# Optimization experiments

Measured on AMD Instinct MI355X. Metric: run time of the kernel, lower is better.

Reference implementation:

```python
import jax, jax.numpy as jnp
import numpy as np

BS = 8
SP_IN, DN_IN = 256, 128
SP_OUT, DN_OUT = 512, 256
N_STK, N_STK_PNT = 32, 64
COOR = 64
SP_NEAR, DN_NEAR = 2, 10
BN_EPS = 1e-5


def _act(x):
    return jax.nn.leaky_relu(x, 0.2)


def _bn(x, g, b, axes):
    # training-mode batch norm over `axes`, per channel (axis 1)
    m = x.mean(axes, keepdims=True)
    v = x.var(axes, keepdims=True)
    shp = [1] * x.ndim
    shp[1] = x.shape[1]
    return g.reshape(shp) * (x - m) * jax.lax.rsqrt(v + BN_EPS) + b.reshape(shp)


def _conv2d(x, w, b, stride, pad_w):
    # x [B,C,H,W], w [O,I,1,kw]
    y = jax.lax.conv_general_dilated(
        x, w, window_strides=stride, padding=[(0, 0), (pad_w, pad_w)],
        dimension_numbers=('NCHW', 'OIHW', 'NCHW'))
    return y + b[None, :, None, None]


def _sq_dist(a, b):
    # a [B,N,C], b [B,M,C] -> [B,N,M]
    return (jnp.sum(a * a, -1)[:, :, None] + jnp.sum(b * b, -1)[:, None, :]
            - 2.0 * jnp.einsum('bnc,bmc->bnm', a, b))


def _index_points(p, idx):
    # p [B,N,C], idx [B,...] -> [B,...,C]
    B = p.shape[0]
    bidx = jnp.arange(B).reshape((B,) + (1,) * (idx.ndim - 1))
    return p[bidx, idx]


def _fps(x, m):
    # deterministic farthest point sampling, start at index 0. x [B,N,D] -> [B,m]
    B, N, _ = x.shape
    bar = jnp.arange(B)

    def step(carry, _):
        dist, far = carry
        cen = x[bar, far]                       # [B,D]
        d = jnp.sum((x - cen[:, None, :]) ** 2, -1)
        dist = jnp.minimum(dist, d)
        return (dist, jnp.argmax(dist, -1).astype(jnp.int32)), far

    init = (jnp.full((B, N), 1e10, x.dtype), jnp.zeros((B,), jnp.int32))
    _, idx = jax.lax.scan(step, init, None, length=m)
    return idx.T  # [B,m]


def _gcn(x, W, b, g, be, k):
    # DGCNN-style EdgeConv: knn in feature space, edge feat [x_j - x_i, x_i],
    # shared 1x1 conv + BN + act, max over neighbors. x [B,C,N] -> [B,O,N]
    xt = jnp.transpose(x, (0, 2, 1))            # [B,N,C]
    d = _sq_dist(xt, xt)
    _, idx = jax.lax.top_k(-d, k)               # [B,N,k] (includes self)
    neigh = _index_points(xt, idx)              # [B,N,k,C]
    cen = xt[:, :, None, :]
    edge = jnp.concatenate([neigh - cen, jnp.broadcast_to(cen, neigh.shape)], -1)
    h = jnp.einsum('bnkc,oc->bonk', edge, W) + b[None, :, None, None]
    h = _act(_bn(h, g, be, (0, 2, 3)))
    return jnp.max(h, axis=3)                   # [B,O,N]


def _forward(sparse_fea, dense_fea, stk_coor,
             d2s_w, d2s_b, d2s_g, d2s_be,
             gsp_w, gsp_b, gsp_g, gsp_be,
             gdn_w, gdn_b, gdn_g, gdn_be,
             dcv_w, dcv_b, dcv_g, dcv_be):
    bs = sparse_fea.shape[0]
    dn4 = dense_fea.reshape(bs, DN_IN, N_STK, N_STK_PNT)

    # DenseToSparse: conv (1,3) valid, BN, act, max over points -> concat
    h = _act(_bn(_conv2d(dn4, d2s_w, d2s_b, (1, 1), 0), d2s_g, d2s_be, (0, 2, 3)))
    sp_from_dn = jnp.max(h, axis=3)                       # [bs,DN_IN,N_STK]
    union_sparse = jnp.concatenate([sparse_fea, sp_from_dn], 1)

    # SparseToDense: broadcast stroke feature onto its points -> concat
    dn_from_sp = jnp.repeat(sparse_fea[:, :, :, None], N_STK_PNT, axis=3)
    union_dense = jnp.concatenate([dn4, dn_from_sp], 1).reshape(
        bs, SP_IN + DN_IN, N_STK * N_STK_PNT)

    # graph updates
    union_sparse = _gcn(union_sparse, gsp_w, gsp_b, gsp_g, gsp_be, SP_NEAR)   # [bs,SP_OUT,N_STK]
    union_dense = _gcn(union_dense, gdn_w, gdn_b, gdn_g, gdn_be, DN_NEAR)     # [bs,DN_OUT,N_pnt]

    # DownSample: FPS over strokes, gather, strided conv halves point count
    fps_idx = _fps(stk_coor, N_STK // 2)                  # [bs,N_STK//2]
    stk_coor_s = _index_points(stk_coor, fps_idx)         # [bs,N_STK//2,COOR]
    sp = jnp.transpose(_index_points(jnp.transpose(union_sparse, (0, 2, 1)), fps_idx), (0, 2, 1))

    emb_d = union_dense.shape[1]
    dn = union_dense.reshape(bs, emb_d, N_STK, N_STK_PNT).transpose(0, 2, 3, 1)
    dn = dn.reshape(bs, N_STK, N_STK_PNT * emb_d)
    dn = _index_points(dn, fps_idx)                       # gather whole strokes
    dn = dn.reshape(bs, N_STK // 2, N_STK_PNT, emb_d).transpose(0, 3, 1, 2)
    dn = _act(_bn(_conv2d(dn, dcv_w, dcv_b, (1, 2), 1), dcv_g, dcv_be, (0, 2, 3)))
    dn = dn.reshape(bs, dn.shape[1], (N_STK // 2) * (N_STK_PNT // 2))
    return sp, dn, stk_coor_s


def setup_inputs() -> dict:
    key = jax.random.key(0)
    ks = jax.random.split(key, 8)
    C_u = SP_IN + DN_IN

    def rn(k, shape, s=0.05):
        return jax.random.normal(k, shape, jnp.float32) * s

    return {
        'sparse_fea': jax.random.normal(ks[0], (BS, SP_IN, N_STK), jnp.float32),
        'dense_fea': jax.random.normal(ks[1], (BS, DN_IN, N_STK * N_STK_PNT), jnp.float32),
        'stk_coor': jax.random.normal(ks[2], (BS, N_STK, COOR), jnp.float32),
        'd2s_w': rn(ks[3], (DN_IN, DN_IN, 1, 3)), 'd2s_b': jnp.zeros(DN_IN),
        'd2s_g': jnp.ones(DN_IN), 'd2s_be': jnp.zeros(DN_IN),
        'gsp_w': rn(ks[4], (SP_OUT, 2 * C_u)), 'gsp_b': jnp.zeros(SP_OUT),
        'gsp_g': jnp.ones(SP_OUT), 'gsp_be': jnp.zeros(SP_OUT),
        'gdn_w': rn(ks[5], (DN_OUT, 2 * C_u)), 'gdn_b': jnp.zeros(DN_OUT),
        'gdn_g': jnp.ones(DN_OUT), 'gdn_be': jnp.zeros(DN_OUT),
        'dcv_w': rn(ks[6], (DN_OUT, DN_OUT, 1, 3)), 'dcv_b': jnp.zeros(DN_OUT),
        'dcv_g': jnp.ones(DN_OUT), 'dcv_be': jnp.zeros(DN_OUT),
    }


def reference(sparse_fea, dense_fea, stk_coor,
              d2s_w, d2s_b, d2s_g, d2s_be,
              gsp_w, gsp_b, gsp_g, gsp_be,
              gdn_w, gdn_b, gdn_g, gdn_be,
              dcv_w, dcv_b, dcv_g, dcv_be):
    return _forward(sparse_fea, dense_fea, stk_coor,
                    d2s_w, d2s_b, d2s_g, d2s_be,
                    gsp_w, gsp_b, gsp_g, gsp_be,
                    gdn_w, gdn_b, gdn_g, gdn_be,
                    dcv_w, dcv_b, dcv_g, dcv_be)
```

## Files before the change

kernel.cpp:

```cpp
#include <hip/hip_runtime.h>

#define NPTS 2048
#define CUF 384

__device__ __forceinline__ float lrelu(float y){ return y>=0.f ? y : 0.2f*y; }

#define GLD16(g, l) __builtin_amdgcn_global_load_lds( \
    (const __attribute__((address_space(1))) void*)(g), \
    (__attribute__((address_space(3))) void*)(l), 16, 0, 0)

__global__ void k_build_xdn(const float* __restrict__ dense,
                            const float* __restrict__ sparse,
                            float* __restrict__ X){
  int b = blockIdx.y, ch = blockIdx.x;
  int t = threadIdx.x;
  __shared__ float tile[64*128];
  for (int k=0;k<32;k++){
    int f = t + k*256;
    int c = f>>6, j = f&63;
    tile[j*128 + c] = dense[((size_t)b*128 + c)*NPTS + ch*64 + j];
  }
  __syncthreads();
  for (int k=0;k<32;k++){
    int f = t + k*256;
    int j = f>>7, c = f&127;
    X[((size_t)b*NPTS + ch*64 + j)*CUF + c] = tile[f];
  }
  float v = sparse[((size_t)b*256 + t)*32 + ch];
  for (int j=0;j<64;j++) X[((size_t)b*NPTS + ch*64 + j)*CUF + 128 + t] = v;
}

__global__ void k_sn(const float* __restrict__ X, float* __restrict__ sn){
  int g = blockIdx.x*256 + threadIdx.x;
  if (g >= 8*NPTS) return;
  const float* row = X + (size_t)g*CUF;
  float blk[4];
  #pragma unroll
  for (int bI=0;bI<4;bI++){
    const float* p = row + bI*96;
    float r[8];
    #pragma unroll
    for (int l=0;l<8;l++) r[l] = __fmul_rn(p[l], p[l]);
    #pragma unroll 1
    for (int i=8;i<96;i+=8){
      #pragma unroll
      for (int l=0;l<8;l++) r[l] = __fadd_rn(r[l], __fmul_rn(p[i+l], p[i+l]));
    }
    float s01 = __fadd_rn(r[0], r[1]);
    float s23 = __fadd_rn(r[2], r[3]);
    float s45 = __fadd_rn(r[4], r[5]);
    float s67 = __fadd_rn(r[6], r[7]);
    blk[bI] = __fadd_rn(__fadd_rn(s01, s23), __fadd_rn(s45, s67));
  }
  sn[g] = __fadd_rn(__fadd_rn(blk[0], blk[1]), __fadd_rn(blk[2], blk[3]));
}

__global__ __launch_bounds__(256) void k_dist_tri(
    const float* __restrict__ X, float* __restrict__ Dot, int b_base){
  int z = blockIdx.z; int b = b_base + z;
  int t = threadIdx.x;
  int tx = t & 15, ty = t >> 4;
  int idx = blockIdx.x, rb = 0;
  while (idx >= 16 - rb){ idx -= 16 - rb; rb++; }
  int cb = rb + idx;
  __shared__ float U[8448];
  float* Xr = U;
  float* Xc = U + 4096;
  float* Ds = U;
  int r0 = rb*128;
  int c0 = cb*128;
  const size_t xb = (size_t)b*NPTS*CUF;
  const size_t zb = (size_t)z*NPTS*NPTS;

  int wv  = t >> 6;
  int sub = (t & 63) >> 3;
  int gs  = t & 7;
  int rowsA[4]; int swzA[4];
  #pragma unroll
  for (int cc=0;cc<4;cc++){
    int grp = wv*4 + cc;
    int row = grp*8 + sub;
    rowsA[cc] = row;
    swzA[cc] = 4*(gs ^ (row&7));
  }

  float acc[8][8];
  #pragma unroll
  for (int i=0;i<8;i++){
    #pragma unroll
    for (int j=0;j<8;j++) acc[i][j] = 0.f;
  }
  for (int kt=0; kt<12; kt++){
    int k0 = kt*32;
    __syncthreads();
    #pragma unroll
    for (int cc=0;cc<4;cc++){
      int grp = wv*4 + cc;
      GLD16(X + xb + (size_t)(r0+rowsA[cc])*CUF + k0 + swzA[cc], Xr + grp*256);
      GLD16(X + xb + (size_t)(c0+rowsA[cc])*CUF + k0 + swzA[cc], Xc + grp*256);
    }
    __syncthreads();
    #pragma unroll
    for (int kk=0; kk<32; kk+=4){
      int G = kk>>2;
      float4 aa[8], bb[8];
      #pragma unroll
      for (int i=0;i<8;i++){ int r = ty+16*i; aa[i] = *(const float4*)&Xr[r*32 + 4*(G ^ (r&7))]; }
      #pragma unroll
      for (int j=0;j<8;j++){ int r = tx+16*j; bb[j] = *(const float4*)&Xc[r*32 + 4*(G ^ (r&7))]; }
      #pragma unroll
      for (int i=0;i<8;i++){
        #pragma unroll
        for (int j=0;j<8;j++){
          float a_ = acc[i][j];
          a_ = fmaf(aa[i].x, bb[j].x, a_);
          a_ = fmaf(aa[i].y, bb[j].y, a_);
          a_ = fmaf(aa[i].z, bb[j].z, a_);
          a_ = fmaf(aa[i].w, bb[j].w, a_);
          acc[i][j] = a_;
        }
      }
    }
  }
  #pragma unroll
  for (int i=0;i<8;i++){
    size_t rbase = zb + (size_t)(r0 + ty + 16*i)*NPTS + c0;
    #pragma unroll
    for (int j=0;j<8;j++) Dot[rbase + tx + 16*j] = acc[i][j];
  }
  if (rb != cb){
    for (int h=0; h<2; h++){
      __syncthreads();
      #pragma unroll
      for (int i2=0;i2<4;i2++){
        #pragma unroll
        for (int j=0;j<8;j++){
          Ds[(tx+16*j)*65 + ty + 16*i2] = acc[h*4+i2][j];
        }
      }
      __syncthreads();
      for (int e=t; e<128*64; e+=256){
        int col = e>>6, rr = e&63;
        Dot[zb + (size_t)(c0+col)*NPTS + r0 + h*64 + rr] = Ds[col*65 + rr];
      }
    }
  }
}

__global__ __launch_bounds__(256) void k_sel(const float* __restrict__ Dot,
                                             const float* __restrict__ sn,
                                             int* __restrict__ idx, int b_base){
  int t = threadIdx.x;
  int lane = t & 63, w = t >> 6;
  int rglob = blockIdx.x*4 + w;
  int bb = rglob >> 11;
  int r  = rglob & 2047;
  int b  = b_base + bb;
  const float* drow = Dot + ((size_t)bb*NPTS + r)*NPTS;
  const float* snp  = sn + (size_t)b*NPTS;
  float snr = snp[r];
  unsigned long long key[32];
  #pragma unroll
  for (int k=0;k<8;k++){
    int cbase = k*256 + lane*4;
    float4 dd = *(const float4*)&drow[cbase];
    float4 ss = *(const float4*)&snp[cbase];
    float v0 = __fsub_rn(__fadd_rn(snr, ss.x), __fmul_rn(2.0f, dd.x));
    float v1 = __fsub_rn(__fadd_rn(snr, ss.y), __fmul_rn(2.0f, dd.y));
    float v2 = __fsub_rn(__fadd_rn(snr, ss.z), __fmul_rn(2.0f, dd.z));
    float v3 = __fsub_rn(__fadd_rn(snr, ss.w), __fmul_rn(2.0f, dd.w));
    float vv[4] = {v0, v1, v2, v3};
    #pragma unroll
    for (int u=0;u<4;u++){
      unsigned int bits = __float_as_uint(vv[u]);
      unsigned int flip = bits ^ ((unsigned int)((int)bits >> 31) | 0x80000000u);
      key[k*4+u] = ((unsigned long long)flip << 32) | (unsigned int)(cbase + u);
    }
  }
  unsigned long long last = 0ull;
  int out[10];
  #pragma unroll
  for (int q=0;q<10;q++){
    const unsigned long long INF = 0xFFFFFFFFFFFFFFFFull;
    unsigned long long m0[16];
    #pragma unroll
    for (int s=0;s<16;s++){
      unsigned long long a = (key[s]    > last) ? key[s]    : INF;
      unsigned long long c = (key[s+16] > last) ? key[s+16] : INF;
      m0[s] = (c < a) ? c : a;
    }
    #pragma unroll
    for (int s=0;s<8;s++) m0[s] = (m0[s+8] < m0[s]) ? m0[s+8] : m0[s];
    #pragma unroll
    for (int s=0;s<4;s++) m0[s] = (m0[s+4] < m0[s]) ? m0[s+4] : m0[s];
    m0[0] = (m0[2] < m0[0]) ? m0[2] : m0[0];
    m0[1] = (m0[3] < m0[1]) ? m0[3] : m0[1];
    unsigned long long m = (m0[1] < m0[0]) ? m0[1] : m0[0];
    #pragma unroll
    for (int sh=1; sh<64; sh<<=1){
      unsigned long long o = (unsigned long long)__shfl_xor((long long)m, sh, 64);
      m = (o < m) ? o : m;
    }
    last = m;
    out[q] = (int)(m & 0xFFFFFFFFull);
  }
  if (lane == 0){
    int* o = idx + ((size_t)b*NPTS + r)*10;
    #pragma unroll
    for (int q=0;q<10;q++) o[q] = out[q];
  }
}

__global__ void k_prepw(const float* __restrict__ Wsrc, float* __restrict__ Wcat, int Ohalf){
  int g = blockIdx.x*256 + threadIdx.x;
  int total = Ohalf*2*CUF;
  if (g >= total) return;
  int o = g / CUF, c = g % CUF;
  float v;
  if (o < Ohalf) v = Wsrc[(size_t)o*768 + c];
  else { int oo = o - Ohalf; v = Wsrc[(size_t)oo*768 + 384 + c] - Wsrc[(size_t)oo*768 + c]; }
  Wcat[g] = v;
}

__global__ __launch_bounds__(256) void k_gemm_pq2(const float* __restrict__ A, const float* __restrict__ W,
                         const float* __restrict__ bias, float* __restrict__ OUT){
  int b = blockIdx.z, mb = blockIdx.y, ob = blockIdx.x;
  int t = threadIdx.x; int tx = t&15, ty = t>>4;
  __shared__ float Xa[4096];
  __shared__ float Xw[4096];
  int m0 = mb*128, o0 = ob*128;
  float acc[8][8];
  #pragma unroll
  for (int i=0;i<8;i++){
    #pragma unroll
    for (int j=0;j<8;j++) acc[i][j] = 0.f;
  }
  int wv  = t >> 6;
  int sub = (t & 63) >> 3;
  int gs  = t & 7;
  int rowsA[4]; int swzA[4];
  #pragma unroll
  for (int cc=0;cc<4;cc++){
    int grp = wv*4 + cc;
    int row = grp*8 + sub;
    rowsA[cc] = row;
    swzA[cc] = 4*(gs ^ (row&7));
  }
  for (int kt=0; kt<12; kt++){
    int k0 = kt*32;
    __syncthreads();
    #pragma unroll
    for (int cc=0;cc<4;cc++){
      int grp = wv*4 + cc;
      GLD16(A + ((size_t)b*NPTS + m0 + rowsA[cc])*CUF + k0 + swzA[cc], Xa + grp*256);
      GLD16(W + (size_t)(o0 + rowsA[cc])*CUF + k0 + swzA[cc], Xw + grp*256);
    }
    __syncthreads();
    #pragma unroll
    for (int kk=0; kk<32; kk+=4){
      int G = kk>>2;
      float4 aa[8], bb[8];
      #pragma unroll
      for (int i=0;i<8;i++){ int r = ty+16*i; aa[i] = *(const float4*)&Xa[r*32 + 4*(G ^ (r&7))]; }
      #pragma unroll
      for (int j=0;j<8;j++){ int r = tx+16*j; bb[j] = *(const float4*)&Xw[r*32 + 4*(G ^ (r&7))]; }
      #pragma unroll
      for (int i=0;i<8;i++){
        #pragma unroll
        for (int j=0;j<8;j++){
          float a_ = acc[i][j];
          a_ = fmaf(aa[i].x, bb[j].x, a_);
          a_ = fmaf(aa[i].y, bb[j].y, a_);
          a_ = fmaf(aa[i].z, bb[j].z, a_);
          a_ = fmaf(aa[i].w, bb[j].w, a_);
          acc[i][j] = a_;
        }
      }
    }
  }
  #pragma unroll
  for (int i=0;i<8;i++){
    int m = m0 + ty + 16*i;
    #pragma unroll
    for (int j=0;j<8;j++){
      int o = o0 + tx + 16*j;
      float v = acc[i][j];
      if (o >= 256) v += bias[o - 256];
      OUT[((size_t)b*NPTS + m)*512 + o] = v;
    }
  }
}

__global__ __launch_bounds__(256) void k_gemm_pq(const float* __restrict__ A, const float* __restrict__ W,
                         const float* __restrict__ bias,
                         float* __restrict__ OUT, int M, int Ototal, int Ohalf){
  int b = blockIdx.z, mb = blockIdx.y, ob = blockIdx.x;
  int t = threadIdx.x; int tr = t&15, tc = t>>4;
  __shared__ float At[64][68], Wt[64][68];
  int m0 = mb*64, o0 = ob*64;
  float acc[4][4];
  #pragma unroll
  for(int i=0;i<4;i++){
    #pragma unroll
    for(int j=0;j<4;j++) acc[i][j]=0.f;
  }
  int li = t>>2, lk = (t&3)*16;
  for (int kt=0;kt<6;kt++){
    int k0 = kt*64;
    {
      int m = m0 + li;
      if (m < M){
        const float4* p = (const float4*)(A + ((size_t)b*M + m)*CUF + k0 + lk);
        #pragma unroll
        for (int e=0;e<4;e++) *(float4*)&At[li][lk+e*4] = p[e];
      } else {
        float4 z = make_float4(0.f,0.f,0.f,0.f);
        #pragma unroll
        for (int e=0;e<4;e++) *(float4*)&At[li][lk+e*4] = z;
      }
      const float4* pw = (const float4*)(W + (size_t)(o0+li)*CUF + k0 + lk);
      #pragma unroll
      for (int e=0;e<4;e++) *(float4*)&Wt[li][lk+e*4] = pw[e];
    }
    __syncthreads();
    #pragma unroll
    for (int k4=0;k4<16;k4++){
      float4 aa[4], bb[4];
      aa[0] = *(const float4*)&At[tr   ][k4*4];
      aa[1] = *(const float4*)&At[tr+16][k4*4];
      aa[2] = *(const float4*)&At[tr+32][k4*4];
      aa[3] = *(const float4*)&At[tr+48][k4*4];
      bb[0] = *(const float4*)&Wt[tc   ][k4*4];
      bb[1] = *(const float4*)&Wt[tc+16][k4*4];
      bb[2] = *(const float4*)&Wt[tc+32][k4*4];
      bb[3] = *(const float4*)&Wt[tc+48][k4*4];
      #pragma unroll
      for(int i=0;i<4;i++){
        #pragma unroll
        for(int j=0;j<4;j++)
          acc[i][j] += aa[i].x*bb[j].x + aa[i].y*bb[j].y + aa[i].z*bb[j].z + aa[i].w*bb[j].w;
      }
    }
    __syncthreads();
  }
  #pragma unroll
  for(int i=0;i<4;i++){
    int m = m0 + tr + 16*i;
    if (m < M){
      #pragma unroll
      for(int j=0;j<4;j++){
        int o = o0 + tc + 16*j;
        float v = acc[i][j];
        if (o >= Ohalf) v += bias[o - Ohalf];
        OUT[((size_t)b*M + m)*Ototal + o] = v;
      }
    }
  }
}

__global__ __launch_bounds__(256) void k_gather_dn(const float* __restrict__ PQ, const int* __restrict__ idx,
                            float* __restrict__ dmax, float* __restrict__ dmin, double* __restrict__ part){
  int b = blockIdx.y, nb = blockIdx.x; int t = threadIdx.x;
  __shared__ int sidx[640];
  int n0 = nb*64;
  for (int k=t; k<640; k+=256) sidx[k] = idx[((size_t)b*NPTS + n0)*10 + k] & 2047;
  __syncthreads();
  double s=0.0, s2=0.0;
  const size_t pb = (size_t)b*NPTS*512;
  for (int n=0;n<64;n++){
    float qv = PQ[pb + (size_t)(n0+n)*512 + 256 + t];
    float mx = -3.4e38f, mn = 3.4e38f;
    #pragma unroll
    for (int k=0;k<10;k++){
      int m = sidx[n*10+k];
      float h = PQ[pb + (size_t)m*512 + t] + qv;
      mx = fmaxf(mx,h); mn = fminf(mn,h);
      s += h; s2 += (double)h*(double)h;
    }
    dmax[((size_t)b*NPTS + n0+n)*256 + t] = mx;
    dmin[((size_t)b*NPTS + n0+n)*256 + t] = mn;
  }
  size_t blk = (size_t)b*32 + nb;
  part[(blk*256 + t)*2] = s; part[(blk*256 + t)*2+1] = s2;
}

__global__ void k_reduce(const double* __restrict__ part, float* __restrict__ mv,
                         int nblk, int C, int count){
  int c = blockIdx.x; int t = threadIdx.x;
  double s=0.0, s2=0.0;
  for (int k=t;k<nblk;k+=64){ s += part[((size_t)k*C+c)*2]; s2 += part[((size_t)k*C+c)*2+1]; }
  #pragma unroll
  for (int off=32; off>=1; off>>=1){ s += __shfl_down(s, off, 64); s2 += __shfl_down(s2, off, 64); }
  if (t==0){
    double mean = s / (double)count;
    double var = s2 / (double)count - mean*mean;
    mv[c*2] = (float)mean;
    mv[c*2+1] = (float)(1.0 / sqrt(var + 1e-5));
  }
}

__global__ void k_epi(const float* __restrict__ xmin, float* __restrict__ xmax,
                      const float* __restrict__ mv, const float* __restrict__ g,
                      const float* __restrict__ be, int C, size_t total){
  size_t i = (size_t)blockIdx.x*256 + threadIdx.x;
  if (i>=total) return;
  int c = (int)(i % (size_t)C);
  float gg = g[c];
  float x = gg >= 0.f ? xmax[i] : xmin[i];
  float y = gg*(x - mv[c*2])*mv[c*2+1] + be[c];
  xmax[i] = lrelu(y);
}

__global__ __launch_bounds__(128) void k_d2s(const float* __restrict__ dense,
                      const float* __restrict__ w, const float* __restrict__ bias,
                      float* __restrict__ mx, float* __restrict__ mn, double* __restrict__ part){
  int b = blockIdx.y, s = blockIdx.x; int t = threadIdx.x;
  __shared__ float IN[128*64];
  for (int k=0;k<64;k++){
    int f = t + k*128;
    int ci = f>>6, wj = f&63;
    IN[f] = dense[((size_t)b*128 + ci)*NPTS + s*64 + wj];
  }
  __syncthreads();
  float acc[62];
  float bv = bias[t];
  #pragma unroll
  for (int wj=0;wj<62;wj++) acc[wj]=bv;
  for (int ci=0;ci<128;ci++){
    const float* wp = w + ((size_t)t*128 + ci)*3;
    float w0 = wp[0], w1 = wp[1], w2 = wp[2];
    const float* row = &IN[ci*64];
    #pragma unroll
    for (int wj=0;wj<62;wj++) acc[wj] += row[wj]*w0 + row[wj+1]*w1 + row[wj+2]*w2;
  }
  float vmx=-3.4e38f, vmn=3.4e38f; double ss=0.0, ss2=0.0;
  #pragma unroll
  for (int wj=0;wj<62;wj++){ float v = acc[wj]; vmx=fmaxf(vmx,v); vmn=fminf(vmn,v); ss+=v; ss2+=(double)v*(double)v; }
  mx[((size_t)b*32+s)*128 + t] = vmx;
  mn[((size_t)b*32+s)*128 + t] = vmn;
  part[(((size_t)b*32+s)*128 + t)*2] = ss; part[(((size_t)b*32+s)*128 + t)*2+1] = ss2;
}

__global__ void k_build_xs(const float* __restrict__ sparse,
                           const float* __restrict__ mx, const float* __restrict__ mn,
                           const float* __restrict__ mv, const float* __restrict__ g,
                           const float* __restrict__ be, float* __restrict__ Xs){
  int b = blockIdx.x; int c = threadIdx.x;
  for (int n=0;n<32;n++){
    float v;
    if (c < 256) v = sparse[((size_t)b*256 + c)*32 + n];
    else {
      int cc = c-256;
      float gg = g[cc];
      float x = gg>=0.f ? mx[((size_t)b*32+n)*128+cc] : mn[((size_t)b*32+n)*128+cc];
      v = lrelu(gg*(x - mv[cc*2])*mv[cc*2+1] + be[cc]);
    }
    Xs[((size_t)b*32+n)*384 + c] = v;
  }
}

__global__ __launch_bounds__(256) void k_knn_sp(const float* __restrict__ Xs, int* __restrict__ idx){
  int b = blockIdx.x; int t = threadIdx.x;
  __shared__ float Xh[32*388];
  __shared__ float snl[32];
  __shared__ float D[32*33];
  for (int k=t;k<32*384;k+=256){ int n=k/384, c=k-n*384; Xh[n*388+c] = Xs[(size_t)b*32*384 + k]; }
  __syncthreads();
  if (t<32){ double s=0.0; for (int c=0;c<384;c++){ double v=(double)Xh[t*388+c]; s+=v*v; } snl[t]=(float)s; }
  __syncthreads();
  for (int p=t;p<1024;p+=256){
    int n=p>>5, m=p&31;
    const float* A=&Xh[n*388]; const float* B=&Xh[m*388];
    double s=0.0;
    for (int c=0;c<384;c++) s += (double)A[c]*(double)B[c];
    D[n*33+m] = (float)((double)snl[m] - 2.0*s);
  }
  __syncthreads();
  if (t<32){
    float v0=3.4e38f,v1=3.4e38f; int i0=0,i1=0;
    for (int m=0;m<32;m++){
      float v=D[t*33+m];
      if (v < v0){ v1=v0;i1=i0; v0=v;i0=m; }
      else if (v < v1){ v1=v;i1=m; }
    }
    idx[((size_t)b*32+t)*2]=i0; idx[((size_t)b*32+t)*2+1]=i1;
  }
}

__global__ void k_gather_sp(const float* __restrict__ PQ, const int* __restrict__ idx,
                            float* __restrict__ umax, float* __restrict__ umin, double* __restrict__ part){
  int b = blockIdx.x; int t = threadIdx.x;
  double s=0.0, s2=0.0;
  for (int n=0;n<32;n++){
    float qv = PQ[((size_t)b*32+n)*1024 + 512 + t];
    float mxv=-3.4e38f, mnv=3.4e38f;
    #pragma unroll
    for (int k=0;k<2;k++){
      int m = idx[((size_t)b*32+n)*2+k] & 31;
      float h = PQ[((size_t)b*32+m)*1024 + t] + qv;
      mxv=fmaxf(mxv,h); mnv=fminf(mnv,h); s+=h; s2+=(double)h*(double)h;
    }
    umax[((size_t)b*32+n)*512+t]=mxv; umin[((size_t)b*32+n)*512+t]=mnv;
  }
  part[((size_t)b*512+t)*2]=s; part[((size_t)b*512+t)*2+1]=s2;
}

__global__ void k_fps(const float* __restrict__ coor, int* __restrict__ fps){
  int b = blockIdx.x; int t = threadIdx.x;
  __shared__ float C[32*64]; __shared__ float dist[32]; __shared__ int fs;
  for (int k=t;k<2048;k+=64) C[k] = coor[(size_t)b*2048 + k];
  if (t<32) dist[t]=1e10f;
  if (t==0) fs=0;
  __syncthreads();
  for (int it=0; it<16; it++){
    int f = fs;
    if (t==0) fps[b*16+it] = f;
    if (t<32){
      float d=0.f;
      for (int c=0;c<64;c++){ float df = C[t*64+c]-C[f*64+c]; d += df*df; }
      dist[t] = fminf(dist[t], d);
    }
    __syncthreads();
    if (t==0){
      float bd=-1.f; int bi=0;
      for (int n=0;n<32;n++){ if (dist[n]>bd){bd=dist[n];bi=n;} }
      fs=bi;
    }
    __syncthreads();
  }
}

__global__ void k_out0(const float* __restrict__ usp, const int* __restrict__ fps, float* __restrict__ out0){
  int b = blockIdx.y, s = blockIdx.x; int t = threadIdx.x;
  int n = fps[b*16+s] & 31;
  out0[((size_t)b*512 + t)*16 + s] = usp[((size_t)b*32+n)*512 + t];
}
__global__ void k_out2(const float* __restrict__ coor, const int* __restrict__ fps, float* __restrict__ out2){
  int b = blockIdx.x; int t = threadIdx.x;
  for (int e=t; e<1024; e+=256){
    int s=e>>6, c=e&63;
    out2[(size_t)b*1024 + e] = coor[((size_t)b*32 + (fps[b*16+s]&31))*64 + c];
  }
}

__global__ __launch_bounds__(256) void k_dcv(const float* __restrict__ gdn, const int* __restrict__ fps,
                      const float* __restrict__ w, const float* __restrict__ bias,
                      float* __restrict__ pre, double* __restrict__ part){
  int s = blockIdx.x, qg = blockIdx.y, b = blockIdx.z; int t = threadIdx.x;
  __shared__ float I[17*256];
  int n0 = (fps[b*16+s] & 31)*64;
  const size_t gbase = ((size_t)b*NPTS + n0)*256;
  for (int e=t; e<17*256; e+=256){
    int lp = e>>8, c = e&255;
    int p = 16*qg - 1 + lp;
    I[e] = (p >= 0) ? gdn[gbase + (size_t)p*256 + c] : 0.f;
  }
  __syncthreads();
  float acc[8];
  float bv = bias[t];
  #pragma unroll
  for (int q=0;q<8;q++) acc[q]=bv;
  for (int ci=0; ci<256; ci+=4){
    float wv[4][3];
    const float* wp = w + ((size_t)t*256 + ci)*3;
    #pragma unroll
    for (int u=0;u<4;u++){ wv[u][0]=wp[u*3]; wv[u][1]=wp[u*3+1]; wv[u][2]=wp[u*3+2]; }
    #pragma unroll
    for (int q=0;q<8;q++){
      float4 a0 = *(const float4*)&I[(2*q  )*256 + ci];
      float4 a1 = *(const float4*)&I[(2*q+1)*256 + ci];
      float4 a2 = *(const float4*)&I[(2*q+2)*256 + ci];
      acc[q] += a0.x*wv[0][0] + a0.y*wv[1][0] + a0.z*wv[2][0] + a0.w*wv[3][0];
      acc[q] += a1.x*wv[0][1] + a1.y*wv[1][1] + a1.z*wv[2][1] + a1.w*wv[3][1];
      acc[q] += a2.x*wv[0][2] + a2.y*wv[1][2] + a2.z*wv[2][2] + a2.w*wv[3][2];
    }
  }
  double ss=0.0, ss2=0.0;
  #pragma unroll
  for (int q=0;q<8;q++){ ss += acc[q]; ss2 += (double)acc[q]*(double)acc[q]; }
  float* o = pre + (((size_t)b*256 + t)*16 + s)*32 + qg*8;
  #pragma unroll
  for (int q=0;q<8;q++) o[q] = acc[q];
  size_t blk = ((size_t)b*16 + s)*4 + qg;
  part[(blk*256 + t)*2] = ss; part[(blk*256 + t)*2+1] = ss2;
}

__global__ void k_epi_dcv(const float* __restrict__ pre, const float* __restrict__ mv,
                          const float* __restrict__ g, const float* __restrict__ be,
                          float* __restrict__ out1){
  size_t i = (size_t)blockIdx.x*256 + threadIdx.x;
  int c = (int)((i>>9) & 255);
  float gg = g[c];
  float y = gg*(pre[i]-mv[c*2])*mv[c*2+1] + be[c];
  out1[i] = lrelu(y);
}

extern "C" void kernel_launch(void* const* d_in, const int* in_sizes, int n_in,
                              void* d_out, int out_size, void* d_ws, size_t ws_size,
                              hipStream_t stream){
  const float* sparse = (const float*)d_in[0];
  const float* dense  = (const float*)d_in[1];
  const float* coor   = (const float*)d_in[2];
  const float* d2s_w  = (const float*)d_in[3];
  const float* d2s_b  = (const float*)d_in[4];
  const float* d2s_g  = (const float*)d_in[5];
  const float* d2s_be = (const float*)d_in[6];
  const float* gsp_w  = (const float*)d_in[7];
  const float* gsp_b  = (const float*)d_in[8];
  const float* gsp_g  = (const float*)d_in[9];
  const float* gsp_be = (const float*)d_in[10];
  const float* gdn_w  = (const float*)d_in[11];
  const float* gdn_b  = (const float*)d_in[12];
  const float* gdn_g  = (const float*)d_in[13];
  const float* gdn_be = (const float*)d_in[14];
  const float* dcv_w  = (const float*)d_in[15];
  const float* dcv_b  = (const float*)d_in[16];
  const float* dcv_g  = (const float*)d_in[17];
  const float* dcv_be = (const float*)d_in[18];

  float* out0 = (float*)d_out;
  float* out1 = out0 + 8*512*16;
  float* out2 = out1 + (size_t)8*256*512;

  char* base = (char*)d_ws; size_t off = 0;
  auto alloc = [&](size_t bytes)->void*{ void* p = base + off; off += (bytes + 255) & ~(size_t)255; return p; };
  float* Xdn  = (float*)alloc((size_t)8*2048*384*4);
  float* sn   = (float*)alloc((size_t)8*2048*4);
  int*   idxd = (int*)alloc((size_t)8*2048*10*4);
  float* PQ   = (float*)alloc((size_t)8*2048*512*4);
  float* dmax = (float*)alloc((size_t)8*2048*256*4);
  float* dmin = (float*)alloc((size_t)8*2048*256*4);
  double* partdn = (double*)alloc((size_t)256*256*2*8);
  float* mvdn = (float*)alloc(256*2*4);
  float* Wcd  = (float*)alloc((size_t)512*384*4);
  float* Wcs  = (float*)alloc((size_t)1024*384*4);
  float* Xs   = (float*)alloc((size_t)8*32*384*4);
  int*   idxs = (int*)alloc(8*32*2*4);
  float* PQs  = (float*)alloc((size_t)8*32*1024*4);
  float* umax = (float*)alloc((size_t)8*32*512*4);
  float* umin = (float*)alloc((size_t)8*32*512*4);
  double* partsp = (double*)alloc((size_t)8*512*2*8);
  float* mvsp = (float*)alloc(512*2*4);
  float* d2mx = (float*)alloc((size_t)8*32*128*4);
  float* d2mn = (float*)alloc((size_t)8*32*128*4);
  double* partd2 = (double*)alloc((size_t)256*128*2*8);
  float* mvd2 = (float*)alloc(128*2*4);
  int* fps = (int*)alloc(8*16*4);
  float* dcvpre = (float*)alloc((size_t)8*256*512*4);
  double* partdcv = (double*)alloc((size_t)512*256*2*8);
  float* mvdcv = (float*)alloc(256*2*4);
  if (off > ws_size) return;

  float* Dot = PQ;

  k_build_xdn<<<dim3(32,8), 256, 0, stream>>>(dense, sparse, Xdn);
  k_sn<<<64, 256, 0, stream>>>(Xdn, sn);
  k_dist_tri<<<dim3(136,1,4), 256, 0, stream>>>(Xdn, Dot, 0);
  k_sel<<<2048, 256, 0, stream>>>(Dot, sn, idxd, 0);
  k_dist_tri<<<dim3(136,1,4), 256, 0, stream>>>(Xdn, Dot, 4);
  k_sel<<<2048, 256, 0, stream>>>(Dot, sn, idxd, 4);
  k_prepw<<<768, 256, 0, stream>>>(gdn_w, Wcd, 256);
  k_prepw<<<1536, 256, 0, stream>>>(gsp_w, Wcs, 512);
  k_gemm_pq2<<<dim3(4,16,8), 256, 0, stream>>>(Xdn, Wcd, gdn_b, PQ);
  k_gather_dn<<<dim3(32,8), 256, 0, stream>>>(PQ, idxd, dmax, dmin, partdn);
  k_reduce<<<256, 64, 0, stream>>>(partdn, mvdn, 256, 256, 163840);
  k_epi<<<16384, 256, 0, stream>>>(dmin, dmax, mvdn, gdn_g, gdn_be, 256, (size_t)8*2048*256);
  k_d2s<<<dim3(32,8), 128, 0, stream>>>(dense, d2s_w, d2s_b, d2mx, d2mn, partd2);
  k_reduce<<<128, 64, 0, stream>>>(partd2, mvd2, 256, 128, 15872);
  k_build_xs<<<8, 384, 0, stream>>>(sparse, d2mx, d2mn, mvd2, d2s_g, d2s_be, Xs);
  k_knn_sp<<<8, 256, 0, stream>>>(Xs, idxs);
  k_gemm_pq<<<dim3(16,1,8), 256, 0, stream>>>(Xs, Wcs, gsp_b, PQs, 32, 1024, 512);
  k_gather_sp<<<8, 512, 0, stream>>>(PQs, idxs, umax, umin, partsp);
  k_reduce<<<512, 64, 0, stream>>>(partsp, mvsp, 8, 512, 512);
  k_epi<<<512, 256, 0, stream>>>(umin, umax, mvsp, gsp_g, gsp_be, 512, (size_t)8*32*512);
  k_fps<<<8, 64, 0, stream>>>(coor, fps);
  k_out0<<<dim3(16,8), 512, 0, stream>>>(umax, fps, out0);
  k_out2<<<8, 256, 0, stream>>>(coor, fps, out2);
  k_dcv<<<dim3(16,4,8), 256, 0, stream>>>(dmax, fps, dcv_w, dcv_b, dcvpre, partdcv);
  k_reduce<<<256, 64, 0, stream>>>(partdcv, mvdcv, 512, 256, 4096);
  k_epi_dcv<<<4096, 256, 0, stream>>>(dcvpre, mvdcv, dcv_g, dcv_be, out1);
}
```

Measured before the change: 760.2 us.

## Process all batches in one distance/select pass and merge small launches

When the workspace can hold the full 8-batch distance matrix, the distance and top-k select kernels run once over all batches instead of in two halves of four. The two weight-prep kernels are merged into one launch, and the two output-gather kernels are merged into one. The shared-memory transpose stride changes from 65 to 67. The aim is fewer kernel launches and larger grids that fill the GPU better, at the cost of a 128 MB scratch buffer; if the workspace is too small, the code falls back to the old two-pass path.

Result: faster. 695.3 us (-8.5%).

```diff
diff --git a/kernel.cpp b/kernel.cpp
--- a/kernel.cpp
+++ b/kernel.cpp
@@ -63,7 +63,7 @@
   int idx = blockIdx.x, rb = 0;
   while (idx >= 16 - rb){ idx -= 16 - rb; rb++; }
   int cb = rb + idx;
-  __shared__ float U[8448];
+  __shared__ float U[8576];
   float* Xr = U;
   float* Xc = U + 4096;
   float* Ds = U;
@@ -135,13 +135,13 @@
       for (int i2=0;i2<4;i2++){
         #pragma unroll
         for (int j=0;j<8;j++){
-          Ds[(tx+16*j)*65 + ty + 16*i2] = acc[h*4+i2][j];
+          Ds[(tx+16*j)*67 + ty + 16*i2] = acc[h*4+i2][j];
         }
       }
       __syncthreads();
       for (int e=t; e<128*64; e+=256){
         int col = e>>6, rr = e&63;
-        Dot[zb + (size_t)(c0+col)*NPTS + r0 + h*64 + rr] = Ds[col*65 + rr];
+        Dot[zb + (size_t)(c0+col)*NPTS + r0 + h*64 + rr] = Ds[col*67 + rr];
       }
     }
   }
@@ -211,15 +211,25 @@
   }
 }
 
-__global__ void k_prepw(const float* __restrict__ Wsrc, float* __restrict__ Wcat, int Ohalf){
+__global__ void k_prepw2(const float* __restrict__ gdn_w, const float* __restrict__ gsp_w,
+                         float* __restrict__ Wcd, float* __restrict__ Wcs){
   int g = blockIdx.x*256 + threadIdx.x;
-  int total = Ohalf*2*CUF;
-  if (g >= total) return;
-  int o = g / CUF, c = g % CUF;
-  float v;
-  if (o < Ohalf) v = Wsrc[(size_t)o*768 + c];
-  else { int oo = o - Ohalf; v = Wsrc[(size_t)oo*768 + 384 + c] - Wsrc[(size_t)oo*768 + c]; }
-  Wcat[g] = v;
+  if (g < 512*CUF){
+    int o = g / CUF, c = g % CUF;
+    float v;
+    if (o < 256) v = gdn_w[(size_t)o*768 + c];
+    else { int oo = o - 256; v = gdn_w[(size_t)oo*768 + 384 + c] - gdn_w[(size_t)oo*768 + c]; }
+    Wcd[g] = v;
+  } else {
+    int g2 = g - 512*CUF;
+    if (g2 < 1024*CUF){
+      int o = g2 / CUF, c = g2 % CUF;
+      float v;
+      if (o < 512) v = gsp_w[(size_t)o*768 + c];
+      else { int oo = o - 512; v = gsp_w[(size_t)oo*768 + 384 + c] - gsp_w[(size_t)oo*768 + c]; }
+      Wcs[g2] = v;
+    }
+  }
 }
 
 __global__ __launch_bounds__(256) void k_gemm_pq2(const float* __restrict__ A, const float* __restrict__ W,
@@ -530,16 +540,19 @@
   }
 }
 
-__global__ void k_out0(const float* __restrict__ usp, const int* __restrict__ fps, float* __restrict__ out0){
-  int b = blockIdx.y, s = blockIdx.x; int t = threadIdx.x;
-  int n = fps[b*16+s] & 31;
-  out0[((size_t)b*512 + t)*16 + s] = usp[((size_t)b*32+n)*512 + t];
-}
-__global__ void k_out2(const float* __restrict__ coor, const int* __restrict__ fps, float* __restrict__ out2){
-  int b = blockIdx.x; int t = threadIdx.x;
-  for (int e=t; e<1024; e+=256){
-    int s=e>>6, c=e&63;
-    out2[(size_t)b*1024 + e] = coor[((size_t)b*32 + (fps[b*16+s]&31))*64 + c];
+__global__ void k_outs(const float* __restrict__ usp, const float* __restrict__ coor,
+                       const int* __restrict__ fps, float* __restrict__ out0, float* __restrict__ out2){
+  int g = blockIdx.x*256 + threadIdx.x;
+  if (g < 65536){
+    int b = g >> 13; int rem = g & 8191; int t = rem >> 4; int s = rem & 15;
+    int n = fps[b*16+s] & 31;
+    out0[((size_t)b*512 + t)*16 + s] = usp[((size_t)b*32+n)*512 + t];
+  } else {
+    int e = g - 65536;
+    if (e < 8192){
+      int b = e >> 10; int r = e & 1023; int s = r>>6, c = r&63;
+      out2[(size_t)b*1024 + r] = coor[((size_t)b*32 + (fps[b*16+s]&31))*64 + c];
+    }
   }
 }
 
@@ -651,16 +664,22 @@
   float* mvdcv = (float*)alloc(256*2*4);
   if (off > ws_size) return;
 
-  float* Dot = PQ;
+  size_t dotBytes = (size_t)8*NPTS*NPTS*4;
+  float* Dot8 = (off + dotBytes <= ws_size) ? (float*)(base + off) : nullptr;
+  float* Dot4 = PQ;
 
   k_build_xdn<<<dim3(32,8), 256, 0, stream>>>(dense, sparse, Xdn);
   k_sn<<<64, 256, 0, stream>>>(Xdn, sn);
-  k_dist_tri<<<dim3(136,1,4), 256, 0, stream>>>(Xdn, Dot, 0);
-  k_sel<<<2048, 256, 0, stream>>>(Dot, sn, idxd, 0);
-  k_dist_tri<<<dim3(136,1,4), 256, 0, stream>>>(Xdn, Dot, 4);
-  k_sel<<<2048, 256, 0, stream>>>(Dot, sn, idxd, 4);
-  k_prepw<<<768, 256, 0, stream>>>(gdn_w, Wcd, 256);
-  k_prepw<<<1536, 256, 0, stream>>>(gsp_w, Wcs, 512);
+  if (Dot8){
+    k_dist_tri<<<dim3(136,1,8), 256, 0, stream>>>(Xdn, Dot8, 0);
+    k_sel<<<4096, 256, 0, stream>>>(Dot8, sn, idxd, 0);
+  } else {
+    k_dist_tri<<<dim3(136,1,4), 256, 0, stream>>>(Xdn, Dot4, 0);
+    k_sel<<<2048, 256, 0, stream>>>(Dot4, sn, idxd, 0);
+    k_dist_tri<<<dim3(136,1,4), 256, 0, stream>>>(Xdn, Dot4, 4);
+    k_sel<<<2048, 256, 0, stream>>>(Dot4, sn, idxd, 4);
+  }
+  k_prepw2<<<2304, 256, 0, stream>>>(gdn_w, gsp_w, Wcd, Wcs);
   k_gemm_pq2<<<dim3(4,16,8), 256, 0, stream>>>(Xdn, Wcd, gdn_b, PQ);
   k_gather_dn<<<dim3(32,8), 256, 0, stream>>>(PQ, idxd, dmax, dmin, partdn);
   k_reduce<<<256, 64, 0, stream>>>(partdn, mvdn, 256, 256, 163840);
@@ -674,8 +693,7 @@
   k_reduce<<<512, 64, 0, stream>>>(partsp, mvsp, 8, 512, 512);
   k_epi<<<512, 256, 0, stream>>>(umin, umax, mvsp, gsp_g, gsp_be, 512, (size_t)8*32*512);
   k_fps<<<8, 64, 0, stream>>>(coor, fps);
-  k_out0<<<dim3(16,8), 512, 0, stream>>>(umax, fps, out0);
-  k_out2<<<8, 256, 0, stream>>>(coor, fps, out2);
+  k_outs<<<288, 256, 0, stream>>>(umax, coor, fps, out0, out2);
   k_dcv<<<dim3(16,4,8), 256, 0, stream>>>(dmax, fps, dcv_w, dcv_b, dcvpre, partdcv);
   k_reduce<<<256, 64, 0, stream>>>(partdcv, mvdcv, 512, 256, 4096);
   k_epi_dcv<<<4096, 256, 0, stream>>>(dcvpre, mvdcv, dcv_g, dcv_be, out1);
```
